# Kernel tuning notes

Hardware: AMD Instinct MI355X
Metric: run time of the kernel (lower is better)

## Reference

```python
import jax, jax.numpy as jnp
import numpy as np

T, B, IN_DIM = 8192, 4, 512
D_V, D_K, CHUNK = 512, 64, 128
EPS = 1e-8


def setup_inputs() -> dict:
    key = jax.random.key(0)
    ks = jax.random.split(key, 9)
    s = 0.02
    return {
        "x": jax.random.normal(ks[0], (T, B, IN_DIM), jnp.float32),
        "Wv": jax.random.normal(ks[1], (D_V, IN_DIM), jnp.float32) * s,
        "bv": jnp.zeros((D_V,), jnp.float32),
        "Wk": jax.random.normal(ks[2], (D_K, IN_DIM), jnp.float32) * s,
        "bk": jnp.zeros((D_K,), jnp.float32),
        "Wq": jax.random.normal(ks[3], (D_K, IN_DIM), jnp.float32) * s,
        "bq": jnp.zeros((D_K,), jnp.float32),
        "Wa": jax.random.normal(ks[4], (D_K, IN_DIM), jnp.float32) * s,
        "ba": jnp.zeros((D_K,), jnp.float32),
    }


def reference(x, Wv, bv, Wk, bk, Wq, bq, Wa, ba):
    # Projections: x (T, B, in_dim)
    v = x @ Wv.T + bv                      # (T, B, d)
    k = x @ Wk.T + bk                      # (T, B, n)
    q = x @ Wq.T + bq                      # (T, B, n)
    alpha = jax.nn.sigmoid(x @ Wa.T + ba)  # (T, B, n) decay gates

    Tt, Bb = x.shape[0], x.shape[1]
    C = CHUNK
    nC = Tt // C  # T assumed divisible by chunk size

    def to_chunks(a):
        return a.reshape(nC, C, Bb, a.shape[-1])

    vs, ks_, qs, als = to_chunks(v), to_chunks(k), to_chunks(q), to_chunks(alpha)
    causal = jnp.tril(jnp.ones((C, C), dtype=bool))  # (C, C)

    def body(S, inp):
        v_ch, k_ch, q_ch, a_ch = inp  # each (C, B, .)
        # Cumulative decay product within chunk (clamped as in the original)
        p = jnp.cumprod(jnp.maximum(a_ch, EPS), axis=0)      # (C, B, n)
        q_t = q_ch * p                                        # (C, B, n)
        k_t = k_ch / (p + EPS)                                # (C, B, n)
        # Intra-chunk causal attention scores
        A = jnp.einsum('tbn,sbn->bts', q_t, k_t)              # (B, C, C)
        A = jnp.where(causal[None, :, :], A, jnp.zeros((), A.dtype))
        y = jnp.einsum('bts,sbd->tbd', A, v_ch)               # intra-chunk
        y = y + jnp.einsum('bdn,tbn->tbd', S, q_t)            # cross-chunk carry
        # State update to end of chunk
        p_end = p[-1]                                         # (B, n)
        S_writes = jnp.einsum('tbd,tbn->bdn', v_ch, k_t * p_end[None, :, :])
        S_new = S * p_end[:, None, :] + S_writes              # (B, d, n)
        return S_new, y

    S0 = jnp.zeros((Bb, D_V, D_K), x.dtype)
    _, ys = jax.lax.scan(body, S0, (vs, ks_, qs, als))        # ys: (nC, C, B, d)
    return ys.reshape(Tt, Bb, D_V)
```

## Files before the change

### kernel.cpp

```cpp
#include <hip/hip_runtime.h>
#include <math.h>

#define T_DIM 8192
#define B_DIM 4
#define INDIM 512
#define DV 512
#define DK 64
#define CHUNK 128
#define NCH (T_DIM / CHUNK)
#define ROWS (T_DIM * B_DIM)
#define NPAD 768
#define KCAT 192
#define EPSF 1e-8f

typedef float float4_t __attribute__((ext_vector_type(4)));
typedef short short8_t __attribute__((ext_vector_type(8)));
typedef _Float16 half8_t __attribute__((ext_vector_type(8)));

__device__ inline unsigned short f2bf(float f) {
  unsigned int u = __float_as_uint(f);
  unsigned int r = (u + 0x7fffu + ((u >> 16) & 1u)) >> 16;
  return (unsigned short)r;
}
__device__ inline float bf2f(unsigned short h) {
  return __uint_as_float(((unsigned int)h) << 16);
}
__device__ inline unsigned short f2h(float f) {
  _Float16 h = (_Float16)f;
  unsigned short u;
  __builtin_memcpy(&u, &h, 2);
  return u;
}

__device__ inline void gload16(const void* g, void* l) {
  __builtin_amdgcn_global_load_lds(
      (const __attribute__((address_space(1))) void*)g,
      (__attribute__((address_space(3))) void*)l, 16, 0, 0);
}

__global__ __launch_bounds__(256) void cast_kernel(
    const float* __restrict__ x,
    const float* __restrict__ Wv, const float* __restrict__ Wk,
    const float* __restrict__ Wq, const float* __restrict__ Wa,
    const float* __restrict__ bv, const float* __restrict__ bk,
    const float* __restrict__ bq, const float* __restrict__ ba,
    unsigned short* __restrict__ xh, unsigned short* __restrict__ wh,
    float* __restrict__ bcat)
{
  if (blockIdx.x < 16384) {
    const size_t i4 = ((size_t)blockIdx.x * 256 + threadIdx.x) * 4;
    const float4 v = *(const float4*)&x[i4];
    ushort4 h;
    h.x = f2h(v.x); h.y = f2h(v.y); h.z = f2h(v.z); h.w = f2h(v.w);
    *(ushort4*)&xh[i4] = h;
  } else {
    const int t = (blockIdx.x - 16384) * 256 + threadIdx.x;
    const size_t i4 = (size_t)t * 4;
    const int row = (int)(i4 >> 9);
    const int col = (int)(i4 & 511);
    float4 v = {0.f, 0.f, 0.f, 0.f};
    if (row < 512)      v = *(const float4*)&Wv[(size_t)row * INDIM + col];
    else if (row < 576) v = *(const float4*)&Wk[(size_t)(row - 512) * INDIM + col];
    else if (row < 640) v = *(const float4*)&Wq[(size_t)(row - 576) * INDIM + col];
    else if (row < 704) v = *(const float4*)&Wa[(size_t)(row - 640) * INDIM + col];
    ushort4 h;
    h.x = f2h(v.x); h.y = f2h(v.y); h.z = f2h(v.z); h.w = f2h(v.w);
    *(ushort4*)&wh[i4] = h;
    if (t < NPAD) {
      float b = 0.f;
      if (t < 512)      b = bv[t];
      else if (t < 576) b = bk[t - 512];
      else if (t < 640) b = bq[t - 576];
      else if (t < 704) b = ba[t - 640];
      bcat[t] = b;
    }
  }
}

__global__ __launch_bounds__(256) void proj_mfma_kernel(
    const unsigned short* __restrict__ xh, const unsigned short* __restrict__ wh,
    const float* __restrict__ bcat,
    float* __restrict__ v_ws, float* __restrict__ k_ws,
    float* __restrict__ q_ws, float* __restrict__ a_ws)
{
  __shared__ __align__(16) _Float16 Ah[2][128 * 32];
  __shared__ __align__(16) _Float16 Bh[2][128 * 32];

  const int d     = blockIdx.x;
  const int grp   = d >> 3;
  const int ytile = (d & 7) * 32 + grp / 6;
  const int xtile = grp % 6;
  const int r0 = ytile * 128;
  const int c0 = xtile * 128;

  const int tid  = threadIdx.x;
  const int wave = tid >> 6, lane = tid & 63;
  const int wm   = (wave & 1) * 64, wn = (wave >> 1) * 64;
  const int fm   = lane & 15;
  const int fk   = (lane >> 4) * 8;

  float4_t acc[4][4];
#pragma unroll
  for (int i = 0; i < 4; ++i)
#pragma unroll
    for (int j = 0; j < 4; ++j) acc[i][j] = (float4_t)0.0f;

  const int srow = tid >> 2;
  const int scol = (tid & 3) * 8;

  const unsigned short* pA0 = xh + (size_t)(r0 + srow) * INDIM + scol;
  const unsigned short* pA1 = xh + (size_t)(r0 + 64 + srow) * INDIM + scol;
  const unsigned short* pB0 = wh + (size_t)(c0 + srow) * INDIM + scol;
  const unsigned short* pB1 = wh + (size_t)(c0 + 64 + srow) * INDIM + scol;

  auto stage = [&](int buf, int k0) {
    gload16(pA0 + k0, &Ah[buf][tid * 8]);
    gload16(pA1 + k0, &Ah[buf][(256 + tid) * 8]);
    gload16(pB0 + k0, &Bh[buf][tid * 8]);
    gload16(pB1 + k0, &Bh[buf][(256 + tid) * 8]);
  };

  auto compute = [&](int buf) {
    half8_t a[4], b[4];
#pragma unroll
    for (int i = 0; i < 4; ++i)
      a[i] = *(const half8_t*)&Ah[buf][(wm + i * 16 + fm) * 32 + fk];
#pragma unroll
    for (int j = 0; j < 4; ++j)
      b[j] = *(const half8_t*)&Bh[buf][(wn + j * 16 + fm) * 32 + fk];
#pragma unroll
    for (int i = 0; i < 4; ++i)
#pragma unroll
      for (int j = 0; j < 4; ++j)
        acc[i][j] = __builtin_amdgcn_mfma_f32_16x16x32_f16(a[i], b[j], acc[i][j], 0, 0, 0);
  };

  stage(0, 0);
  int cur = 0;
  for (int t = 0; t < 15; ++t) {
    stage(cur ^ 1, (t + 1) * 32);
    asm volatile("s_waitcnt vmcnt(4)" ::: "memory");
    __builtin_amdgcn_s_barrier();
    compute(cur);
    __builtin_amdgcn_s_barrier();
    cur ^= 1;
  }
  asm volatile("s_waitcnt vmcnt(0)" ::: "memory");
  __builtin_amdgcn_s_barrier();
  compute(cur);

#pragma unroll
  for (int j = 0; j < 4; ++j) {
    const int col = c0 + wn + j * 16 + fm;
    if (col >= 704) continue;
    const float bias = bcat[col];
#pragma unroll
    for (int i = 0; i < 4; ++i) {
#pragma unroll
      for (int r = 0; r < 4; ++r) {
        const int row = r0 + wm + i * 16 + (lane >> 4) * 4 + r;
        const float val = acc[i][j][r] + bias;
        if (col < 512) {
          v_ws[(size_t)row * DV + col] = val;
        } else if (col < 576) {
          k_ws[(size_t)row * DK + col - 512] = val;
        } else if (col < 640) {
          q_ws[(size_t)row * DK + col - 576] = val;
        } else {
          a_ws[(size_t)row * DK + col - 640] = 1.0f / (1.0f + expf(-val));
        }
      }
    }
  }
}

__global__ __launch_bounds__(256) void prep_kernel(
    const float* __restrict__ a_ws, float* __restrict__ k_ws,
    const float* __restrict__ q_ws,
    unsigned short* __restrict__ Acat_h, unsigned short* __restrict__ Acat_l,
    float* __restrict__ pend)
{
  __shared__ float pal[CHUNK][DK];
  const int c = blockIdx.x, b = blockIdx.y;
  const int cb = c * B_DIM + b;
  const int tid = threadIdx.x;

#pragma unroll
  for (int i = 0; i < 8; ++i) {
    const int f = (i * 256 + tid) * 4;
    const int t = f >> 6, n0 = f & 63;
    const float4 av = *(const float4*)&a_ws[(size_t)(c * CHUNK + t) * 256 + b * 64 + n0];
    *(float4*)&pal[t][n0] = av;
  }
  __syncthreads();

  if (tid < 64) {
    float p = 1.0f;
#pragma unroll 4
    for (int t = 0; t < CHUNK; ++t) {
      p *= fmaxf(pal[t][tid], EPSF);
      pal[t][tid] = p;
    }
    pend[c * 256 + b * 64 + tid] = p;
  }
  __syncthreads();

#pragma unroll
  for (int i = 0; i < 8; ++i) {
    const int f = (i * 256 + tid) * 4;
    const int t = f >> 6, n0 = f & 63;
    const float4 qv = *(const float4*)&q_ws[(size_t)(c * CHUNK + t) * 256 + b * 64 + n0];
    const size_t qa = ((size_t)cb * CHUNK + t) * KCAT + 128 + n0;
    float q0 = qv.x * pal[t][n0 + 0];
    float q1 = qv.y * pal[t][n0 + 1];
    float q2 = qv.z * pal[t][n0 + 2];
    float q3 = qv.w * pal[t][n0 + 3];
    ushort4 h, l;
    h.x = f2bf(q0); l.x = f2bf(q0 - bf2f(h.x));
    h.y = f2bf(q1); l.y = f2bf(q1 - bf2f(h.y));
    h.z = f2bf(q2); l.z = f2bf(q2 - bf2f(h.z));
    h.w = f2bf(q3); l.w = f2bf(q3 - bf2f(h.w));
    *(ushort4*)&Acat_h[qa] = h;
    *(ushort4*)&Acat_l[qa] = l;
  }

#pragma unroll
  for (int i = 0; i < 8; ++i) {
    const int f = (i * 256 + tid) * 4;
    const int t = f >> 6, n0 = f & 63;
    const size_t ka = (size_t)(c * CHUNK + t) * 256 + b * 64 + n0;
    float4 kv = *(const float4*)&k_ws[ka];
    kv.x = kv.x / (pal[t][n0 + 0] + EPSF);
    kv.y = kv.y / (pal[t][n0 + 1] + EPSF);
    kv.z = kv.z / (pal[t][n0 + 2] + EPSF);
    kv.w = kv.w / (pal[t][n0 + 3] + EPSF);
    *(float4*)&k_ws[ka] = kv;
  }
}

__global__ __launch_bounds__(256) void vt_kernel(
    const float* __restrict__ v_ws,
    unsigned short* __restrict__ Bt_h, unsigned short* __restrict__ Bt_l)
{
  __shared__ float Ts[CHUNK][65];
  const int c = blockIdx.x, b = blockIdx.y, dblk = blockIdx.z;
  const int cb = c * B_DIM + b;
  const int d0 = dblk * 64;
  const int tid = threadIdx.x;
#pragma unroll
  for (int q = 0; q < 8; ++q) {
    const int idx = (q * 256 + tid) * 4;
    const int s = idx >> 6, dd = idx & 63;
    const float4 v = *(const float4*)&v_ws[(size_t)((c * CHUNK + s) * B_DIM + b) * DV + d0 + dd];
    Ts[s][dd + 0] = v.x; Ts[s][dd + 1] = v.y;
    Ts[s][dd + 2] = v.z; Ts[s][dd + 3] = v.w;
  }
  __syncthreads();
#pragma unroll
  for (int q = 0; q < 8; ++q) {
    const int idx = (q * 256 + tid) * 4;
    const int dd = idx >> 7, s0 = idx & 127;
    float v0 = Ts[s0 + 0][dd], v1 = Ts[s0 + 1][dd];
    float v2 = Ts[s0 + 2][dd], v3 = Ts[s0 + 3][dd];
    ushort4 h, l;
    h.x = f2bf(v0); l.x = f2bf(v0 - bf2f(h.x));
    h.y = f2bf(v1); l.y = f2bf(v1 - bf2f(h.y));
    h.z = f2bf(v2); l.z = f2bf(v2 - bf2f(h.z));
    h.w = f2bf(v3); l.w = f2bf(v3 - bf2f(h.w));
    const size_t oa = ((size_t)cb * DV + d0 + dd) * CHUNK + s0;
    *(ushort4*)&Bt_h[oa] = h;
    *(ushort4*)&Bt_l[oa] = l;
  }
}

__global__ __launch_bounds__(256) void wchunk_mfma_kernel(
    const unsigned short* __restrict__ Bt_h, const unsigned short* __restrict__ Bt_l,
    const float* __restrict__ k_ws, const float* __restrict__ pend,
    float* __restrict__ W_ws)
{
  __shared__ __align__(16) unsigned short Ah[128 * 32];
  __shared__ __align__(16) unsigned short Al[128 * 32];

  const int c = blockIdx.x, b = blockIdx.y, dt = blockIdx.z;
  const int cb = c * B_DIM + b;
  const int tid  = threadIdx.x;
  const int wave = tid >> 6, lane = tid & 63;
  const int wm   = (wave & 1) * 64;
  const int wn   = (wave >> 1) * 32;
  const int fm   = lane & 15;
  const int fk   = (lane >> 4) * 8;

  const unsigned short* Ab_h = Bt_h + ((size_t)cb * DV + dt * 128) * CHUNK;
  const unsigned short* Ab_l = Bt_l + ((size_t)cb * DV + dt * 128) * CHUNK;

  float4_t acc[4][2];
#pragma unroll
  for (int i = 0; i < 4; ++i)
#pragma unroll
    for (int j = 0; j < 2; ++j) acc[i][j] = (float4_t)0.0f;

  for (int ks = 0; ks < 4; ++ks) {
    const int k0 = ks * 32;
#pragma unroll
    for (int q = 0; q < 2; ++q) {
      const int flat = (q * 256 + tid) * 8;
      const int row = flat >> 5, col = flat & 31;
      gload16(&Ab_h[(size_t)row * CHUNK + k0 + col], &Ah[flat]);
      gload16(&Ab_l[(size_t)row * CHUNK + k0 + col], &Al[flat]);
    }

    short8_t b_hi[2], b_lo[2];
#pragma unroll
    for (int j = 0; j < 2; ++j) {
      const int n = wn + j * 16 + fm;
#pragma unroll
      for (int e = 0; e < 8; ++e) {
        const float kv = k_ws[(size_t)(c * CHUNK + k0 + fk + e) * 256 + b * 64 + n];
        const unsigned short h = f2bf(kv);
        b_hi[j][e] = (short)h;
        b_lo[j][e] = (short)f2bf(kv - bf2f(h));
      }
    }
    __syncthreads();

    short8_t a_hi[4], a_lo[4];
#pragma unroll
    for (int i = 0; i < 4; ++i) {
      const int ar = (wm + i * 16 + fm) * 32 + fk;
      a_hi[i] = *(const short8_t*)&Ah[ar];
      a_lo[i] = *(const short8_t*)&Al[ar];
    }
#pragma unroll
    for (int i = 0; i < 4; ++i)
#pragma unroll
      for (int j = 0; j < 2; ++j) {
        acc[i][j] = __builtin_amdgcn_mfma_f32_16x16x32_bf16(a_hi[i], b_hi[j], acc[i][j], 0, 0, 0);
        acc[i][j] = __builtin_amdgcn_mfma_f32_16x16x32_bf16(a_lo[i], b_hi[j], acc[i][j], 0, 0, 0);
        acc[i][j] = __builtin_amdgcn_mfma_f32_16x16x32_bf16(a_hi[i], b_lo[j], acc[i][j], 0, 0, 0);
      }
    __syncthreads();
  }

#pragma unroll
  for (int j = 0; j < 2; ++j) {
    const int n = wn + j * 16 + fm;
    const float pj = pend[c * 256 + b * 64 + n];
#pragma unroll
    for (int i = 0; i < 4; ++i) {
#pragma unroll
      for (int r = 0; r < 4; ++r) {
        const int d = dt * 128 + wm + i * 16 + (lane >> 4) * 4 + r;
        W_ws[((size_t)cb * DV + d) * DK + n] = acc[i][j][r] * pj;
      }
    }
  }
}

__global__ __launch_bounds__(256) void scan_kernel(
    float* __restrict__ W_ws, const float* __restrict__ pend)
{
  const int flat = blockIdx.x * 256 + threadIdx.x;
  const int n = flat & 63;
  const int bd = flat >> 6;
  const int b = bd >> 9;
  float s = 0.0f;
  for (int c = 0; c < NCH; ++c) {
    const int off = c * 131072 + flat;
    const float w = W_ws[off];
    W_ws[off] = s;
    s = s * pend[c * 256 + b * 64 + n] + w;
  }
}

__global__ __launch_bounds__(256) void score_mfma_kernel(
    const float* __restrict__ k_ws,
    unsigned short* __restrict__ Acat_h, unsigned short* __restrict__ Acat_l)
{
  __shared__ __align__(16) unsigned short Ah[128 * 32];
  __shared__ __align__(16) unsigned short Al[128 * 32];
  __shared__ __align__(16) unsigned short Bh[128 * 32];
  __shared__ __align__(16) unsigned short Bl[128 * 32];

  const int c = blockIdx.x, b = blockIdx.y;
  const int cb = c * B_DIM + b;
  const int tid  = threadIdx.x;
  const int wave = tid >> 6, lane = tid & 63;
  const int wm   = (wave & 1) * 64, wn = (wave >> 1) * 64;
  const int fm   = lane & 15;
  const int fk   = (lane >> 4) * 8;

  const unsigned short* Aq_h = Acat_h + (size_t)cb * CHUNK * KCAT + 128;
  const unsigned short* Aq_l = Acat_l + (size_t)cb * CHUNK * KCAT + 128;

  float4_t acc[4][4];
#pragma unroll
  for (int i = 0; i < 4; ++i)
#pragma unroll
    for (int j = 0; j < 4; ++j) acc[i][j] = (float4_t)0.0f;

  for (int ks = 0; ks < 2; ++ks) {
    const int k0 = ks * 32;
#pragma unroll
    for (int q = 0; q < 2; ++q) {
      const int flat = (q * 256 + tid) * 8;
      const int row = flat >> 5, col = flat & 31;
      gload16(&Aq_h[(size_t)row * KCAT + k0 + col], &Ah[flat]);
      gload16(&Aq_l[(size_t)row * KCAT + k0 + col], &Al[flat]);
    }
#pragma unroll
    for (int q = 0; q < 4; ++q) {
      const int flat = (q * 256 + tid) * 4;
      const int s = flat >> 5, n0 = flat & 31;
      const float4 kv = *(const float4*)&k_ws[(size_t)(c * CHUNK + s) * 256 + b * 64 + k0 + n0];
      ushort4 h, l;
      h.x = f2bf(kv.x); l.x = f2bf(kv.x - bf2f(h.x));
      h.y = f2bf(kv.y); l.y = f2bf(kv.y - bf2f(h.y));
      h.z = f2bf(kv.z); l.z = f2bf(kv.z - bf2f(h.z));
      h.w = f2bf(kv.w); l.w = f2bf(kv.w - bf2f(h.w));
      *(ushort4*)&Bh[s * 32 + n0] = h;
      *(ushort4*)&Bl[s * 32 + n0] = l;
    }
    __syncthreads();

    short8_t a_hi[4], a_lo[4], b_hi[4], b_lo[4];
#pragma unroll
    for (int i = 0; i < 4; ++i) {
      const int ar = (wm + i * 16 + fm) * 32 + fk;
      a_hi[i] = *(const short8_t*)&Ah[ar];
      a_lo[i] = *(const short8_t*)&Al[ar];
    }
#pragma unroll
    for (int j = 0; j < 4; ++j) {
      const int br = (wn + j * 16 + fm) * 32 + fk;
      b_hi[j] = *(const short8_t*)&Bh[br];
      b_lo[j] = *(const short8_t*)&Bl[br];
    }
#pragma unroll
    for (int i = 0; i < 4; ++i)
#pragma unroll
      for (int j = 0; j < 4; ++j) {
        acc[i][j] = __builtin_amdgcn_mfma_f32_16x16x32_bf16(a_hi[i], b_hi[j], acc[i][j], 0, 0, 0);
        acc[i][j] = __builtin_amdgcn_mfma_f32_16x16x32_bf16(a_lo[i], b_hi[j], acc[i][j], 0, 0, 0);
        acc[i][j] = __builtin_amdgcn_mfma_f32_16x16x32_bf16(a_hi[i], b_lo[j], acc[i][j], 0, 0, 0);
      }
    __syncthreads();
  }

#pragma unroll
  for (int j = 0; j < 4; ++j) {
    const int s = wn + j * 16 + fm;
#pragma unroll
    for (int i = 0; i < 4; ++i) {
#pragma unroll
      for (int r = 0; r < 4; ++r) {
        const int t = wm + i * 16 + (lane >> 4) * 4 + r;
        const float vv = (s <= t) ? acc[i][j][r] : 0.0f;
        const unsigned short h = f2bf(vv);
        const size_t oa = ((size_t)cb * CHUNK + t) * KCAT + s;
        Acat_h[oa] = h;
        Acat_l[oa] = f2bf(vv - bf2f(h));
      }
    }
  }
}

__global__ __launch_bounds__(256) void out_mfma_kernel(
    const unsigned short* __restrict__ Acat_h, const unsigned short* __restrict__ Acat_l,
    const unsigned short* __restrict__ Bt_h, const unsigned short* __restrict__ Bt_l,
    const float* __restrict__ W_ws, float* __restrict__ out)
{
  __shared__ __align__(16) unsigned short Ah[128 * 32];
  __shared__ __align__(16) unsigned short Al[128 * 32];
  __shared__ __align__(16) unsigned short Bh[128 * 32];
  __shared__ __align__(16) unsigned short Bl[128 * 32];

  const int c = blockIdx.x, b = blockIdx.y, nt = blockIdx.z;
  const int cb = c * B_DIM + b;
  const int tid  = threadIdx.x;
  const int wave = tid >> 6, lane = tid & 63;
  const int wm   = (wave & 1) * 64, wn = (wave >> 1) * 64;
  const int fm   = lane & 15;
  const int fk   = (lane >> 4) * 8;

  const unsigned short* Ab_h = Acat_h + (size_t)cb * CHUNK * KCAT;
  const unsigned short* Ab_l = Acat_l + (size_t)cb * CHUNK * KCAT;
  const unsigned short* Bb_h = Bt_h + ((size_t)cb * DV + nt * 128) * CHUNK;
  const unsigned short* Bb_l = Bt_l + ((size_t)cb * DV + nt * 128) * CHUNK;
  const float* Sb = W_ws + ((size_t)cb * DV + nt * 128) * DK;

  float4_t acc[4][4];
#pragma unroll
  for (int i = 0; i < 4; ++i)
#pragma unroll
    for (int j = 0; j < 4; ++j) acc[i][j] = (float4_t)0.0f;

  for (int ks = 0; ks < 6; ++ks) {
    const int k0 = ks * 32;
#pragma unroll
    for (int q = 0; q < 2; ++q) {
      const int flat = q * 2048 + tid * 8;
      const int row = flat >> 5, col = flat & 31;
      gload16(&Ab_h[(size_t)row * KCAT + k0 + col], &Ah[flat]);
      gload16(&Ab_l[(size_t)row * KCAT + k0 + col], &Al[flat]);
    }
    if (ks < 4) {
#pragma unroll
      for (int q = 0; q < 2; ++q) {
        const int flat = q * 2048 + tid * 8;
        const int row = flat >> 5, col = flat & 31;
        gload16(&Bb_h[(size_t)row * CHUNK + k0 + col], &Bh[flat]);
        gload16(&Bb_l[(size_t)row * CHUNK + k0 + col], &Bl[flat]);
      }
    } else {
#pragma unroll
      for (int q = 0; q < 4; ++q) {
        const int flat = (q * 256 + tid) * 4;
        const int r = flat >> 5, n0 = flat & 31;
        const float4 sv = *(const float4*)&Sb[(size_t)r * DK + (k0 - 128) + n0];
        ushort4 h, l;
        h.x = f2bf(sv.x); l.x = f2bf(sv.x - bf2f(h.x));
        h.y = f2bf(sv.y); l.y = f2bf(sv.y - bf2f(h.y));
        h.z = f2bf(sv.z); l.z = f2bf(sv.z - bf2f(h.z));
        h.w = f2bf(sv.w); l.w = f2bf(sv.w - bf2f(h.w));
        *(ushort4*)&Bh[r * 32 + n0] = h;
        *(ushort4*)&Bl[r * 32 + n0] = l;
      }
    }
    __syncthreads();

    short8_t a_hi[4], a_lo[4], b_hi[4], b_lo[4];
#pragma unroll
    for (int i = 0; i < 4; ++i) {
      const int ar = (wm + i * 16 + fm) * 32 + fk;
      a_hi[i] = *(const short8_t*)&Ah[ar];
      a_lo[i] = *(const short8_t*)&Al[ar];
    }
#pragma unroll
    for (int j = 0; j < 4; ++j) {
      const int br = (wn + j * 16 + fm) * 32 + fk;
      b_hi[j] = *(const short8_t*)&Bh[br];
      b_lo[j] = *(const short8_t*)&Bl[br];
    }
#pragma unroll
    for (int i = 0; i < 4; ++i)
#pragma unroll
      for (int j = 0; j < 4; ++j) {
        acc[i][j] = __builtin_amdgcn_mfma_f32_16x16x32_bf16(a_hi[i], b_hi[j], acc[i][j], 0, 0, 0);
        acc[i][j] = __builtin_amdgcn_mfma_f32_16x16x32_bf16(a_lo[i], b_hi[j], acc[i][j], 0, 0, 0);
        acc[i][j] = __builtin_amdgcn_mfma_f32_16x16x32_bf16(a_hi[i], b_lo[j], acc[i][j], 0, 0, 0);
      }
    __syncthreads();
  }

#pragma unroll
  for (int j = 0; j < 4; ++j) {
    const int d = nt * 128 + wn + j * 16 + fm;
#pragma unroll
    for (int i = 0; i < 4; ++i) {
#pragma unroll
      for (int r = 0; r < 4; ++r) {
        const int t = c * CHUNK + wm + i * 16 + (lane >> 4) * 4 + r;
        out[((size_t)t * B_DIM + b) * DV + d] = acc[i][j][r];
      }
    }
  }
}

extern "C" void kernel_launch(void* const* d_in, const int* in_sizes, int n_in,
                              void* d_out, int out_size, void* d_ws, size_t ws_size,
                              hipStream_t stream)
{
  const float* x  = (const float*)d_in[0];
  const float* Wv = (const float*)d_in[1];
  const float* bv = (const float*)d_in[2];
  const float* Wk = (const float*)d_in[3];
  const float* bk = (const float*)d_in[4];
  const float* Wq = (const float*)d_in[5];
  const float* bq = (const float*)d_in[6];
  const float* Wa = (const float*)d_in[7];
  const float* ba = (const float*)d_in[8];
  float* out = (float*)d_out;

  float* ws   = (float*)d_ws;
  float* v_ws = ws;
  float* k_ws = v_ws + (size_t)ROWS * DV;
  float* a_ws = k_ws + (size_t)ROWS * DK;
  float* pend = a_ws + (size_t)ROWS * DK;
  float* W_ws = pend + NCH * B_DIM * DK;
  float* bcat = W_ws + (size_t)NCH * B_DIM * DV * DK;
  unsigned short* Acat_h = (unsigned short*)(bcat + NPAD);
  unsigned short* Acat_l = Acat_h + (size_t)NCH * B_DIM * CHUNK * KCAT;
  unsigned short* uni = Acat_l + (size_t)NCH * B_DIM * CHUNK * KCAT;
  unsigned short* xh = uni;
  unsigned short* wh = xh + (size_t)ROWS * INDIM;
  float* q_ws = (float*)(uni + (size_t)18 * 1024 * 1024);
  unsigned short* Bt_h = uni;
  unsigned short* Bt_l = Bt_h + (size_t)NCH * B_DIM * DV * CHUNK;

  cast_kernel<<<16384 + 384, 256, 0, stream>>>(
      x, Wv, Wk, Wq, Wa, bv, bk, bq, ba, xh, wh, bcat);
  proj_mfma_kernel<<<(ROWS / 128) * (NPAD / 128), 256, 0, stream>>>(
      xh, wh, bcat, v_ws, k_ws, q_ws, a_ws);
  prep_kernel<<<dim3(NCH, B_DIM), 256, 0, stream>>>(
      a_ws, k_ws, q_ws, Acat_h, Acat_l, pend);
  vt_kernel<<<dim3(NCH, B_DIM, 8), 256, 0, stream>>>(v_ws, Bt_h, Bt_l);
  wchunk_mfma_kernel<<<dim3(NCH, B_DIM, 4), 256, 0, stream>>>(
      Bt_h, Bt_l, k_ws, pend, W_ws);
  scan_kernel<<<(B_DIM * DV * DK) / 256, 256, 0, stream>>>(W_ws, pend);
  score_mfma_kernel<<<dim3(NCH, B_DIM), 256, 0, stream>>>(
      k_ws, Acat_h, Acat_l);
  out_mfma_kernel<<<dim3(NCH, B_DIM, 4), 256, 0, stream>>>(
      Acat_h, Acat_l, Bt_h, Bt_l, W_ws, out);
}
```

Before: 308.4 us.

## Triple-buffer projection, pre-split scan state to bf16, swizzle wider LDS tiles

```diff
diff --git a/kernel.cpp b/kernel.cpp
--- a/kernel.cpp
+++ b/kernel.cpp
@@ -83,8 +83,8 @@
     float* __restrict__ v_ws, float* __restrict__ k_ws,
     float* __restrict__ q_ws, float* __restrict__ a_ws)
 {
-  __shared__ __align__(16) _Float16 Ah[2][128 * 32];
-  __shared__ __align__(16) _Float16 Bh[2][128 * 32];
+  __shared__ __align__(16) _Float16 Ah[3][128 * 32];
+  __shared__ __align__(16) _Float16 Bh[3][128 * 32];
 
   const int d     = blockIdx.x;
   const int grp   = d >> 3;
@@ -128,23 +128,30 @@
 #pragma unroll
     for (int j = 0; j < 4; ++j)
       b[j] = *(const half8_t*)&Bh[buf][(wn + j * 16 + fm) * 32 + fk];
+    __builtin_amdgcn_s_setprio(1);
 #pragma unroll
     for (int i = 0; i < 4; ++i)
 #pragma unroll
       for (int j = 0; j < 4; ++j)
         acc[i][j] = __builtin_amdgcn_mfma_f32_16x16x32_f16(a[i], b[j], acc[i][j], 0, 0, 0);
+    __builtin_amdgcn_s_setprio(0);
   };
 
   stage(0, 0);
+  stage(1, 32);
   int cur = 0;
-  for (int t = 0; t < 15; ++t) {
-    stage(cur ^ 1, (t + 1) * 32);
-    asm volatile("s_waitcnt vmcnt(4)" ::: "memory");
+  for (int t = 0; t < 14; ++t) {
+    stage((cur + 2) % 3, (t + 2) * 32);
+    asm volatile("s_waitcnt vmcnt(8)" ::: "memory");
     __builtin_amdgcn_s_barrier();
     compute(cur);
     __builtin_amdgcn_s_barrier();
-    cur ^= 1;
-  }
+    cur = (cur + 1) % 3;
+  }
+  asm volatile("s_waitcnt vmcnt(4)" ::: "memory");
+  __builtin_amdgcn_s_barrier();
+  compute(cur);
+  cur = (cur + 1) % 3;
   asm volatile("s_waitcnt vmcnt(0)" ::: "memory");
   __builtin_amdgcn_s_barrier();
   compute(cur);
@@ -357,7 +364,8 @@
 }
 
 __global__ __launch_bounds__(256) void scan_kernel(
-    float* __restrict__ W_ws, const float* __restrict__ pend)
+    const float* __restrict__ W_ws, const float* __restrict__ pend,
+    unsigned short* __restrict__ Sh, unsigned short* __restrict__ Sl)
 {
   const int flat = blockIdx.x * 256 + threadIdx.x;
   const int n = flat & 63;
@@ -367,7 +375,9 @@
   for (int c = 0; c < NCH; ++c) {
     const int off = c * 131072 + flat;
     const float w = W_ws[off];
-    W_ws[off] = s;
+    const unsigned short h = f2bf(s);
+    Sh[off] = h;
+    Sl[off] = f2bf(s - bf2f(h));
     s = s * pend[c * 256 + b * 64 + n] + w;
   }
 }
@@ -376,10 +386,10 @@
     const float* __restrict__ k_ws,
     unsigned short* __restrict__ Acat_h, unsigned short* __restrict__ Acat_l)
 {
-  __shared__ __align__(16) unsigned short Ah[128 * 32];
-  __shared__ __align__(16) unsigned short Al[128 * 32];
-  __shared__ __align__(16) unsigned short Bh[128 * 32];
-  __shared__ __align__(16) unsigned short Bl[128 * 32];
+  __shared__ __align__(16) unsigned short Ah[128 * 64];
+  __shared__ __align__(16) unsigned short Al[128 * 64];
+  __shared__ __align__(16) unsigned short Bh[128 * 64];
+  __shared__ __align__(16) unsigned short Bl[128 * 64];
 
   const int c = blockIdx.x, b = blockIdx.y;
   const int cb = c * B_DIM + b;
@@ -392,49 +402,57 @@
   const unsigned short* Aq_h = Acat_h + (size_t)cb * CHUNK * KCAT + 128;
   const unsigned short* Aq_l = Acat_l + (size_t)cb * CHUNK * KCAT + 128;
 
+  const int srow = tid >> 3;
+  const int scolB = (tid & 7) * 16;
+  const int sc = (scolB ^ ((srow & 7) << 4)) >> 1;
+  const int sdst = srow * 64 + (scolB >> 1);
+#pragma unroll
+  for (int q = 0; q < 4; ++q) {
+    const int row = q * 32 + srow;
+    const int dst = q * 2048 + sdst;
+    gload16(&Aq_h[(size_t)row * KCAT + sc], &Ah[dst]);
+    gload16(&Aq_l[(size_t)row * KCAT + sc], &Al[dst]);
+  }
+#pragma unroll
+  for (int q = 0; q < 8; ++q) {
+    const int f = (q * 256 + tid) * 4;
+    const int s = f >> 6, n0 = f & 63;
+    const float4 kv = *(const float4*)&k_ws[(size_t)(c * CHUNK + s) * 256 + b * 64 + n0];
+    ushort4 h, l;
+    h.x = f2bf(kv.x); l.x = f2bf(kv.x - bf2f(h.x));
+    h.y = f2bf(kv.y); l.y = f2bf(kv.y - bf2f(h.y));
+    h.z = f2bf(kv.z); l.z = f2bf(kv.z - bf2f(h.z));
+    h.w = f2bf(kv.w); l.w = f2bf(kv.w - bf2f(h.w));
+    const int wi = s * 64 + (n0 ^ ((s & 7) << 3));
+    *(ushort4*)&Bh[wi] = h;
+    *(ushort4*)&Bl[wi] = l;
+  }
+  __syncthreads();
+
   float4_t acc[4][4];
 #pragma unroll
   for (int i = 0; i < 4; ++i)
 #pragma unroll
     for (int j = 0; j < 4; ++j) acc[i][j] = (float4_t)0.0f;
 
-  for (int ks = 0; ks < 2; ++ks) {
-    const int k0 = ks * 32;
-#pragma unroll
-    for (int q = 0; q < 2; ++q) {
-      const int flat = (q * 256 + tid) * 8;
-      const int row = flat >> 5, col = flat & 31;
-      gload16(&Aq_h[(size_t)row * KCAT + k0 + col], &Ah[flat]);
-      gload16(&Aq_l[(size_t)row * KCAT + k0 + col], &Al[flat]);
-    }
-#pragma unroll
-    for (int q = 0; q < 4; ++q) {
-      const int flat = (q * 256 + tid) * 4;
-      const int s = flat >> 5, n0 = flat & 31;
-      const float4 kv = *(const float4*)&k_ws[(size_t)(c * CHUNK + s) * 256 + b * 64 + k0 + n0];
-      ushort4 h, l;
-      h.x = f2bf(kv.x); l.x = f2bf(kv.x - bf2f(h.x));
-      h.y = f2bf(kv.y); l.y = f2bf(kv.y - bf2f(h.y));
-      h.z = f2bf(kv.z); l.z = f2bf(kv.z - bf2f(h.z));
-      h.w = f2bf(kv.w); l.w = f2bf(kv.w - bf2f(h.w));
-      *(ushort4*)&Bh[s * 32 + n0] = h;
-      *(ushort4*)&Bl[s * 32 + n0] = l;
-    }
-    __syncthreads();
-
+#pragma unroll
+  for (int ksub = 0; ksub < 2; ++ksub) {
     short8_t a_hi[4], a_lo[4], b_hi[4], b_lo[4];
 #pragma unroll
     for (int i = 0; i < 4; ++i) {
-      const int ar = (wm + i * 16 + fm) * 32 + fk;
+      const int r = wm + i * 16 + fm;
+      const int ar = r * 64 + ((ksub * 32 + fk) ^ ((r & 7) << 3));
       a_hi[i] = *(const short8_t*)&Ah[ar];
       a_lo[i] = *(const short8_t*)&Al[ar];
     }
 #pragma unroll
     for (int j = 0; j < 4; ++j) {
-      const int br = (wn + j * 16 + fm) * 32 + fk;
+      const int r = wn + j * 16 + fm;
+      const int br = r * 64 + ((ksub * 32 + fk) ^ ((r & 7) << 3));
       b_hi[j] = *(const short8_t*)&Bh[br];
       b_lo[j] = *(const short8_t*)&Bl[br];
     }
+    __builtin_amdgcn_s_setprio(1);
 #pragma unroll
     for (int i = 0; i < 4; ++i)
 #pragma unroll
@@ -443,7 +461,7 @@
         acc[i][j] = __builtin_amdgcn_mfma_f32_16x16x32_bf16(a_lo[i], b_hi[j], acc[i][j], 0, 0, 0);
         acc[i][j] = __builtin_amdgcn_mfma_f32_16x16x32_bf16(a_hi[i], b_lo[j], acc[i][j], 0, 0, 0);
       }
-    __syncthreads();
+    __builtin_amdgcn_s_setprio(0);
   }
 
 #pragma unroll
@@ -467,12 +485,13 @@
 __global__ __launch_bounds__(256) void out_mfma_kernel(
     const unsigned short* __restrict__ Acat_h, const unsigned short* __restrict__ Acat_l,
     const unsigned short* __restrict__ Bt_h, const unsigned short* __restrict__ Bt_l,
-    const float* __restrict__ W_ws, float* __restrict__ out)
-{
-  __shared__ __align__(16) unsigned short Ah[128 * 32];
-  __shared__ __align__(16) unsigned short Al[128 * 32];
-  __shared__ __align__(16) unsigned short Bh[128 * 32];
-  __shared__ __align__(16) unsigned short Bl[128 * 32];
+    const unsigned short* __restrict__ Sh, const unsigned short* __restrict__ Sl,
+    float* __restrict__ out)
+{
+  __shared__ __align__(16) unsigned short Ah[128 * 64];
+  __shared__ __align__(16) unsigned short Al[128 * 64];
+  __shared__ __align__(16) unsigned short Bh[128 * 64];
+  __shared__ __align__(16) unsigned short Bl[128 * 64];
 
   const int c = blockIdx.x, b = blockIdx.y, nt = blockIdx.z;
   const int cb = c * B_DIM + b;
@@ -486,7 +505,13 @@
   const unsigned short* Ab_l = Acat_l + (size_t)cb * CHUNK * KCAT;
   const unsigned short* Bb_h = Bt_h + ((size_t)cb * DV + nt * 128) * CHUNK;
   const unsigned short* Bb_l = Bt_l + ((size_t)cb * DV + nt * 128) * CHUNK;
-  const float* Sb = W_ws + ((size_t)cb * DV + nt * 128) * DK;
+  const unsigned short* Sb_h = Sh + ((size_t)cb * DV + nt * 128) * DK;
+  const unsigned short* Sb_l = Sl + ((size_t)cb * DV + nt * 128) * DK;
+
+  const int srow = tid >> 3;
+  const int scolB = (tid & 7) * 16;
+  const int sc = (scolB ^ ((srow & 7) << 4)) >> 1;
+  const int sdst = srow * 64 + (scolB >> 1);
 
   float4_t acc[4][4];
 #pragma unroll
@@ -494,61 +519,52 @@
 #pragma unroll
     for (int j = 0; j < 4; ++j) acc[i][j] = (float4_t)0.0f;
 
-  for (int ks = 0; ks < 6; ++ks) {
-    const int k0 = ks * 32;
-#pragma unroll
-    for (int q = 0; q < 2; ++q) {
-      const int flat = q * 2048 + tid * 8;
-      const int row = flat >> 5, col = flat & 31;
-      gload16(&Ab_h[(size_t)row * KCAT + k0 + col], &Ah[flat]);
-      gload16(&Ab_l[(size_t)row * KCAT + k0 + col], &Al[flat]);
-    }
-    if (ks < 4) {
-#pragma unroll
-      for (int q = 0; q < 2; ++q) {
-        const int flat = q * 2048 + tid * 8;
-        const int row = flat >> 5, col = flat & 31;
-        gload16(&Bb_h[(size_t)row * CHUNK + k0 + col], &Bh[flat]);
-        gload16(&Bb_l[(size_t)row * CHUNK + k0 + col], &Bl[flat]);
-      }
-    } else {
-#pragma unroll
-      for (int q = 0; q < 4; ++q) {
-        const int flat = (q * 256 + tid) * 4;
-        const int r = flat >> 5, n0 = flat & 31;
-        const float4 sv = *(const float4*)&Sb[(size_t)r * DK + (k0 - 128) + n0];
-        ushort4 h, l;
-        h.x = f2bf(sv.x); l.x = f2bf(sv.x - bf2f(h.x));
-        h.y = f2bf(sv.y); l.y = f2bf(sv.y - bf2f(h.y));
-        h.z = f2bf(sv.z); l.z = f2bf(sv.z - bf2f(h.z));
-        h.w = f2bf(sv.w); l.w = f2bf(sv.w - bf2f(h.w));
-        *(ushort4*)&Bh[r * 32 + n0] = h;
-        *(ushort4*)&Bl[r * 32 + n0] = l;
+  for (int ks = 0; ks < 3; ++ks) {
+    const int k0 = ks * 64;
+#pragma unroll
+    for (int q = 0; q < 4; ++q) {
+      const int row = q * 32 + srow;
+      const int dst = q * 2048 + sdst;
+      gload16(&Ab_h[(size_t)row * KCAT + k0 + sc], &Ah[dst]);
+      gload16(&Ab_l[(size_t)row * KCAT + k0 + sc], &Al[dst]);
+      if (ks < 2) {
+        gload16(&Bb_h[(size_t)row * CHUNK + k0 + sc], &Bh[dst]);
+        gload16(&Bb_l[(size_t)row * CHUNK + k0 + sc], &Bl[dst]);
+      } else {
+        gload16(&Sb_h[(size_t)row * DK + sc], &Bh[dst]);
+        gload16(&Sb_l[(size_t)row * DK + sc], &Bl[dst]);
       }
     }
     __syncthreads();
 
-    short8_t a_hi[4], a_lo[4], b_hi[4], b_lo[4];
-#pragma unroll
-    for (int i = 0; i < 4; ++i) {
-      const int ar = (wm + i * 16 + fm) * 32 + fk;
-      a_hi[i] = *(const short8_t*)&Ah[ar];
-      a_lo[i] = *(const short8_t*)&Al[ar];
-    }
-#pragma unroll
-    for (int j = 0; j < 4; ++j) {
-      const int br = (wn + j * 16 + fm) * 32 + fk;
-      b_hi[j] = *(const short8_t*)&Bh[br];
-      b_lo[j] = *(const short8_t*)&Bl[br];
-    }
-#pragma unroll
-    for (int i = 0; i < 4; ++i)
+#pragma unroll
+    for (int ksub = 0; ksub < 2; ++ksub) {
+      short8_t a_hi[4], a_lo[4], b_hi[4], b_lo[4];
+#pragma unroll
+      for (int i = 0; i < 4; ++i) {
+        const int r = wm + i * 16 + fm;
+        const int ar = r * 64 + ((ksub * 32 + fk) ^ ((r & 7) << 3));
+        a_hi[i] = *(const short8_t*)&Ah[ar];
+        a_lo[i] = *(const short8_t*)&Al[ar];
+      }
 #pragma unroll
       for (int j = 0; j < 4; ++j) {
-        acc[i][j] = __builtin_amdgcn_mfma_f32_16x16x32_bf16(a_hi[i], b_hi[j], acc[i][j], 0, 0, 0);
-        acc[i][j] = __builtin_amdgcn_mfma_f32_16x16x32_bf16(a_lo[i], b_hi[j], acc[i][j], 0, 0, 0);
-        acc[i][j] = __builtin_amdgcn_mfma_f32_16x16x32_bf16(a_hi[i], b_lo[j], acc[i][j], 0, 0, 0);
-      }
+        const int r = wn + j * 16 + fm;
+        const int br = r * 64 + ((ksub * 32 + fk) ^ ((r & 7) << 3));
+        b_hi[j] = *(const short8_t*)&Bh[br];
+        b_lo[j] = *(const short8_t*)&Bl[br];
+      }
+      __builtin_amdgcn_s_setprio(1);
+#pragma unroll
+      for (int i = 0; i < 4; ++i)
+#pragma unroll
+        for (int j = 0; j < 4; ++j) {
+          acc[i][j] = __builtin_amdgcn_mfma_f32_16x16x32_bf16(a_hi[i], b_hi[j], acc[i][j], 0, 0, 0);
+          acc[i][j] = __builtin_amdgcn_mfma_f32_16x16x32_bf16(a_lo[i], b_hi[j], acc[i][j], 0, 0, 0);
+          acc[i][j] = __builtin_amdgcn_mfma_f32_16x16x32_bf16(a_hi[i], b_lo[j], acc[i][j], 0, 0, 0);
+        }
+      __builtin_amdgcn_s_setprio(0);
+    }
     __syncthreads();
   }
 
@@ -596,6 +612,8 @@
   float* q_ws = (float*)(uni + (size_t)18 * 1024 * 1024);
   unsigned short* Bt_h = uni;
   unsigned short* Bt_l = Bt_h + (size_t)NCH * B_DIM * DV * CHUNK;
+  unsigned short* S_h = (unsigned short*)v_ws;
+  unsigned short* S_l = S_h + (size_t)NCH * B_DIM * DV * DK;
 
   cast_kernel<<<16384 + 384, 256, 0, stream>>>(
       x, Wv, Wk, Wq, Wa, bv, bk, bq, ba, xh, wh, bcat);
@@ -606,9 +624,10 @@
   vt_kernel<<<dim3(NCH, B_DIM, 8), 256, 0, stream>>>(v_ws, Bt_h, Bt_l);
   wchunk_mfma_kernel<<<dim3(NCH, B_DIM, 4), 256, 0, stream>>>(
       Bt_h, Bt_l, k_ws, pend, W_ws);
-  scan_kernel<<<(B_DIM * DV * DK) / 256, 256, 0, stream>>>(W_ws, pend);
+  scan_kernel<<<(B_DIM * DV * DK) / 256, 256, 0, stream>>>(
+      W_ws, pend, S_h, S_l);
   score_mfma_kernel<<<dim3(NCH, B_DIM), 256, 0, stream>>>(
       k_ws, Acat_h, Acat_l);
   out_mfma_kernel<<<dim3(NCH, B_DIM, 4), 256, 0, stream>>>(
-      Acat_h, Acat_l, Bt_h, Bt_l, W_ws, out);
-}
+      Acat_h, Acat_l, Bt_h, Bt_l, S_h, S_l, out);
+}
```

Result: no change. 304.0 us (-1.4%).
